# Optimization experiments

Measured on AMD Instinct MI355X. Metric: run time of the kernel, lower is better.

## Reference

```python
import jax, jax.numpy as jnp
import numpy as np

N, E = 50000, 800000
IN, HID, LAT = 512, 256, 128


def setup_inputs() -> dict:
    key = jax.random.key(0)
    ks = jax.random.split(key, 9)
    x = jax.random.normal(ks[0], (N, IN), dtype=jnp.float32)
    edge_index = jax.random.randint(ks[1], (2, E), 0, N, dtype=jnp.int64)
    edge_attr = jax.random.uniform(ks[2], (E,), dtype=jnp.float32)
    # GCNConv weights (glorot-ish scaling) and biases
    W1 = jax.random.normal(ks[3], (IN, HID), dtype=jnp.float32) / np.sqrt(IN)
    b1 = jnp.zeros((HID,), dtype=jnp.float32)
    W_mu = jax.random.normal(ks[4], (HID, LAT), dtype=jnp.float32) / np.sqrt(HID)
    b_mu = jnp.zeros((LAT,), dtype=jnp.float32)
    W_lv = jax.random.normal(ks[5], (HID, LAT), dtype=jnp.float32) / np.sqrt(HID)
    b_lv = jnp.zeros((LAT,), dtype=jnp.float32)
    return {"x": x, "edge_index": edge_index, "edge_attr": edge_attr,
            "W1": W1, "b1": b1, "W_mu": W_mu, "b_mu": b_mu,
            "W_lv": W_lv, "b_lv": b_lv}


def _gcn_norm(edge_index, edge_attr, num_nodes):
    # GCNConv default: add self-loops (weight 1), symmetric normalization
    loops = jnp.arange(num_nodes, dtype=edge_index.dtype)
    src = jnp.concatenate([edge_index[0], loops])
    dst = jnp.concatenate([edge_index[1], loops])
    w = jnp.concatenate([edge_attr, jnp.ones((num_nodes,), edge_attr.dtype)])
    deg = jax.ops.segment_sum(w, dst, num_segments=num_nodes)
    dis = jnp.where(deg > 0, jax.lax.rsqrt(jnp.maximum(deg, 1e-12)), 0.0)
    norm = dis[src] * w * dis[dst]  # [E + N]
    return src, dst, norm


def reference(x, edge_index, edge_attr, W1, b1, W_mu, b_mu, W_lv, b_lv):
    num_nodes = x.shape[0]
    src, dst, norm = _gcn_norm(edge_index, edge_attr, num_nodes)

    def conv(h, W, b):
        m = h @ W                      # dense transform [N, out]
        msg = m[src] * norm[:, None]   # gather + scale  [E+N, out]
        return jax.ops.segment_sum(msg, dst, num_segments=num_nodes) + b

    hidden = jax.nn.relu(conv(x, W1, b1))
    # Dropout(0.2) is identity in eval mode
    mu = conv(hidden, W_mu, b_mu)
    logvar = conv(hidden, W_lv, b_lv)
    return (mu, logvar)
```

## Files before the change

### kernel.cpp

```cpp
#include <hip/hip_runtime.h>

#define IN_F 512
#define HID_F 256
#define LAT_F 128

typedef __bf16 bf16x8 __attribute__((ext_vector_type(8)));
typedef float floatx4 __attribute__((ext_vector_type(4)));

#define FIX_SCALE 1048576.0f

__device__ __forceinline__ unsigned short f2bf(float f) {
    union { float f; unsigned u; } v; v.f = f;
    unsigned r = (v.u + 0x7fff + ((v.u >> 16) & 1)) >> 16;
    return (unsigned short)r;
}
__device__ __forceinline__ float bf2f(unsigned short h) {
    union { unsigned u; float f; } v; v.u = ((unsigned)h) << 16;
    return v.f;
}


__global__ void prep_all(const float* __restrict__ W1, const float* __restrict__ Wmu,
                         const float* __restrict__ Wlv, unsigned long long* __restrict__ packed,
                         unsigned short* __restrict__ Bf1, unsigned short* __restrict__ Bf2,
                         int N) {
    int t = blockIdx.x * 256 + threadIdx.x;
    if (t < N) packed[t] = (1ULL << 32) | (unsigned long long)(unsigned)FIX_SCALE;
    if (t < HID_F * IN_F) {
        int j = t & 7, l = (t >> 3) & 63, jj = (t >> 9) & 1, ks = (t >> 10) & 15, w = t >> 14;
        int n = w * 32 + jj * 16 + (l & 15);
        int k = ks * 32 + (l >> 4) * 8 + j;
        Bf1[t] = f2bf(W1[(size_t)k * HID_F + n]);
    }
    if (t < HID_F * HID_F) {
        int j = t & 7, l = (t >> 3) & 63, jj = (t >> 9) & 1, ks = (t >> 10) & 7, w = t >> 13;
        int n = w * 32 + jj * 16 + (l & 15);
        int k = ks * 32 + (l >> 4) * 8 + j;
        float v = (n < 128) ? Wmu[(size_t)k * LAT_F + n] : Wlv[(size_t)k * LAT_F + (n - 128)];
        Bf2[t] = f2bf(v);
    }
}


__global__ void edge_deg(const int* __restrict__ ei, const float* __restrict__ attr,
                         unsigned long long* __restrict__ packed, int* __restrict__ slot, int E) {
    int e = blockIdx.x * 256 + threadIdx.x;
    if (e < E) {
        int d = ei[E + e];
        unsigned fw = __float2uint_rn(attr[e] * FIX_SCALE);
        unsigned long long old = atomicAdd(&packed[d], (1ULL << 32) | (unsigned long long)fw);
        slot[e] = (int)(old >> 32);
    }
}


__global__ void scan_blocks(const unsigned long long* __restrict__ packed,
                            float* __restrict__ dis, int* __restrict__ excl,
                            int* __restrict__ blockSums, int N) {
    __shared__ int sdata[256];
    int tid = threadIdx.x;
    int base = blockIdx.x * 1024 + tid * 4;
    int v[4]; int sum = 0;
#pragma unroll
    for (int j = 0; j < 4; ++j) {
        int c = 0;
        if (base + j < N) {
            unsigned long long p = packed[base + j];
            c = (int)(p >> 32);
            float dg = (float)(unsigned)(p & 0xffffffffu) * (1.0f / FIX_SCALE);
            dis[base + j] = dg > 0.f ? rsqrtf(fmaxf(dg, 1e-12f)) : 0.f;
        }
        v[j] = c; sum += c;
    }
    sdata[tid] = sum;
    __syncthreads();
    for (int off = 1; off < 256; off <<= 1) {
        int t = (tid >= off) ? sdata[tid - off] : 0;
        __syncthreads();
        sdata[tid] += t;
        __syncthreads();
    }
    if (tid == 255) blockSums[blockIdx.x] = sdata[255];
    int run = sdata[tid] - sum;
#pragma unroll
    for (int j = 0; j < 4; ++j) { if (base + j < N) excl[base + j] = run; run += v[j]; }
}

__global__ void scan_sums(int* blockSums, int NB) {
    __shared__ int s[64];
    int tid = threadIdx.x;
    int v = (tid < NB) ? blockSums[tid] : 0;
    s[tid] = v;
    __syncthreads();
    for (int off = 1; off < 64; off <<= 1) {
        int t = (tid >= off) ? s[tid - off] : 0;
        __syncthreads();
        s[tid] += t;
        __syncthreads();
    }
    if (tid < NB) blockSums[tid] = s[tid] - v;
}

__global__ void scan_add(int* row_ptr, const int* __restrict__ blockSums, int N, int total) {
    int tid = threadIdx.x;
    int base = blockIdx.x * 1024 + tid * 4;
    int add = blockSums[blockIdx.x];
#pragma unroll
    for (int j = 0; j < 4; ++j) if (base + j < N) row_ptr[base + j] += add;
    if (blockIdx.x == 0 && tid == 0) row_ptr[N] = total;
}


__global__ void fill_csr(const int* __restrict__ ei, const float* __restrict__ attr,
                         const int* __restrict__ slot, const float* __restrict__ dis,
                         const int* __restrict__ row_ptr,
                         int* __restrict__ col, float* __restrict__ val, int E, int N) {
    int e = blockIdx.x * 256 + threadIdx.x;
    if (e >= E + N) return;
    int s, d, sl; float w;
    if (e < E) { s = ei[e]; d = ei[E + e]; w = attr[e]; sl = slot[e]; }
    else       { s = d = e - E; w = 1.0f; sl = 0; }
    int pos = row_ptr[d] + sl;
    col[pos] = s;
    val[pos] = dis[s] * w * dis[d];
}


template <bool ABF16, int KK>
__global__ __launch_bounds__(512, 2) void gemm_breg(const void* __restrict__ Avoid,
                                                    const unsigned short* __restrict__ Bfrag,
                                                    unsigned short* __restrict__ C,
                                                    int M, int ntiles) {
    constexpr int NKS = KK / 32;
    constexpr int S   = KK / 128;
    __shared__ unsigned short As[2][64 * 128];

    int tid = threadIdx.x;
    int wave = tid >> 6, lane = tid & 63;
    int mrow = lane & 15, quad = lane >> 4;

    const unsigned short* Abf = (const unsigned short*)Avoid;
    const float*          Afp = (const float*)Avoid;

    bf16x8 bfr[NKS][2];
#pragma unroll
    for (int ks = 0; ks < NKS; ++ks)
#pragma unroll
        for (int jj = 0; jj < 2; ++jj)
            bfr[ks][jj] = *(const bf16x8*)(Bfrag +
                ((((size_t)wave * NKS + ks) * 2 + jj) * 64 + lane) * 8);

    int c  = tid & 15;
    int r0 = tid >> 4;
    int cs0 = (c ^ (r0 & 7)) << 3;
    int cs1 = (c ^ ((r0 + 32) & 7)) << 3;

    float4 a0, a1, a2, a3;
    uint4  u0, u1;

    auto issue = [&](int t_, int s_) {
        int g0 = t_ * 64 + r0;       if (g0 >= M) g0 = M - 1;
        int g1 = t_ * 64 + r0 + 32;  if (g1 >= M) g1 = M - 1;
        if constexpr (ABF16) {
            u0 = *(const uint4*)(Abf + (size_t)g0 * KK + s_ * 128 + c * 8);
            u1 = *(const uint4*)(Abf + (size_t)g1 * KK + s_ * 128 + c * 8);
        } else {
            const float* p0 = Afp + (size_t)g0 * KK + s_ * 128 + c * 8;
            const float* p1 = Afp + (size_t)g1 * KK + s_ * 128 + c * 8;
            a0 = *(const float4*)p0; a1 = *(const float4*)(p0 + 4);
            a2 = *(const float4*)p1; a3 = *(const float4*)(p1 + 4);
        }
    };

    floatx4 acc[4][2];
#pragma unroll
    for (int i = 0; i < 4; ++i)
#pragma unroll
        for (int jj = 0; jj < 2; ++jj) acc[i][jj] = (floatx4){0.f, 0.f, 0.f, 0.f};

    int tile = blockIdx.x;
    if (tile < ntiles) issue(tile, 0);
    int cur = 0;

    for (; tile < ntiles; tile += gridDim.x) {
#pragma unroll
        for (int s = 0; s < S; ++s) {
            if constexpr (ABF16) {
                *(uint4*)&As[cur][r0 * 128 + cs0] = u0;
                *(uint4*)&As[cur][(r0 + 32) * 128 + cs1] = u1;
            } else {
                unsigned short h0[8] = {f2bf(a0.x), f2bf(a0.y), f2bf(a0.z), f2bf(a0.w),
                                        f2bf(a1.x), f2bf(a1.y), f2bf(a1.z), f2bf(a1.w)};
                unsigned short h1[8] = {f2bf(a2.x), f2bf(a2.y), f2bf(a2.z), f2bf(a2.w),
                                        f2bf(a3.x), f2bf(a3.y), f2bf(a3.z), f2bf(a3.w)};
                *(uint4*)&As[cur][r0 * 128 + cs0] = *(uint4*)h0;
                *(uint4*)&As[cur][(r0 + 32) * 128 + cs1] = *(uint4*)h1;
            }
            if (s + 1 < S) issue(tile, s + 1);
            else if (tile + (int)gridDim.x < ntiles) issue(tile + gridDim.x, 0);

            asm volatile("s_waitcnt lgkmcnt(0)" ::: "memory");
            __builtin_amdgcn_s_barrier();

#pragma unroll
            for (int ks = 0; ks < 4; ++ks) {
#pragma unroll
                for (int i = 0; i < 4; ++i) {
                    int row = i * 16 + mrow;
                    bf16x8 af = *(const bf16x8*)&As[cur][row * 128 +
                                    (((ks * 4 + quad) ^ (row & 7)) << 3)];
#pragma unroll
                    for (int jj = 0; jj < 2; ++jj)
                        acc[i][jj] = __builtin_amdgcn_mfma_f32_16x16x32_bf16(
                            af, bfr[s * 4 + ks][jj], acc[i][jj], 0, 0, 0);
                }
            }
            asm volatile("s_waitcnt lgkmcnt(0)" ::: "memory");
            __builtin_amdgcn_s_barrier();
            cur ^= 1;
        }
#pragma unroll
        for (int i = 0; i < 4; ++i)
#pragma unroll
            for (int jj = 0; jj < 2; ++jj) {
                int colo = wave * 32 + jj * 16 + mrow;
#pragma unroll
                for (int v = 0; v < 4; ++v) {
                    int row = tile * 64 + i * 16 + quad * 4 + v;
                    if (row < M) C[(size_t)row * HID_F + colo] = f2bf(acc[i][jj][v]);
                }
                acc[i][jj] = (floatx4){0.f, 0.f, 0.f, 0.f};
            }
    }
}


__global__ void agg_relu(const unsigned short* __restrict__ m, const int* __restrict__ row_ptr,
                         const int* __restrict__ col, const float* __restrict__ val,
                         const float* __restrict__ bias, unsigned short* __restrict__ hidden,
                         int N) {
    int wave = threadIdx.x >> 6, lane = threadIdx.x & 63;
    int i = blockIdx.x * 4 + wave;
    if (i >= N) return;
    int c0 = lane << 2;
    int p0 = __builtin_amdgcn_readfirstlane(row_ptr[i]);
    int p1 = __builtin_amdgcn_readfirstlane(row_ptr[i + 1]);
    float a0 = 0.f, a1 = 0.f, a2 = 0.f, a3 = 0.f;
    for (int p = p0; p < p1; p += 8) {
        int sj[8]; float wj[8];
#pragma unroll
        for (int j = 0; j < 8; ++j) {
            int q = p + j;
            bool ok = q < p1; if (!ok) q = p1 - 1;
            sj[j] = col[q];
            wj[j] = ok ? val[q] : 0.f;
        }
        ushort4 u[8];
#pragma unroll
        for (int j = 0; j < 8; ++j)
            u[j] = *(const ushort4*)(m + (size_t)sj[j] * HID_F + c0);
#pragma unroll
        for (int j = 0; j < 8; ++j) {
            a0 = fmaf(bf2f(u[j].x), wj[j], a0);
            a1 = fmaf(bf2f(u[j].y), wj[j], a1);
            a2 = fmaf(bf2f(u[j].z), wj[j], a2);
            a3 = fmaf(bf2f(u[j].w), wj[j], a3);
        }
    }
    float4 b = *(const float4*)(bias + c0);
    a0 = fmaxf(a0 + b.x, 0.f); a1 = fmaxf(a1 + b.y, 0.f);
    a2 = fmaxf(a2 + b.z, 0.f); a3 = fmaxf(a3 + b.w, 0.f);
    ushort4 o = make_ushort4(f2bf(a0), f2bf(a1), f2bf(a2), f2bf(a3));
    *(ushort4*)(hidden + (size_t)i * HID_F + c0) = o;
}

__global__ void agg_out(const unsigned short* __restrict__ m, const int* __restrict__ row_ptr,
                        const int* __restrict__ col, const float* __restrict__ val,
                        const float* __restrict__ bmu, const float* __restrict__ blv,
                        float* __restrict__ out, int N) {
    int wave = threadIdx.x >> 6, lane = threadIdx.x & 63;
    int i = blockIdx.x * 4 + wave;
    if (i >= N) return;
    int c0 = lane << 2;
    int p0 = __builtin_amdgcn_readfirstlane(row_ptr[i]);
    int p1 = __builtin_amdgcn_readfirstlane(row_ptr[i + 1]);
    float a0 = 0.f, a1 = 0.f, a2 = 0.f, a3 = 0.f;
    for (int p = p0; p < p1; p += 8) {
        int sj[8]; float wj[8];
#pragma unroll
        for (int j = 0; j < 8; ++j) {
            int q = p + j;
            bool ok = q < p1; if (!ok) q = p1 - 1;
            sj[j] = col[q];
            wj[j] = ok ? val[q] : 0.f;
        }
        ushort4 u[8];
#pragma unroll
        for (int j = 0; j < 8; ++j)
            u[j] = *(const ushort4*)(m + (size_t)sj[j] * HID_F + c0);
#pragma unroll
        for (int j = 0; j < 8; ++j) {
            a0 = fmaf(bf2f(u[j].x), wj[j], a0);
            a1 = fmaf(bf2f(u[j].y), wj[j], a1);
            a2 = fmaf(bf2f(u[j].z), wj[j], a2);
            a3 = fmaf(bf2f(u[j].w), wj[j], a3);
        }
    }
    if (lane < 32) {
        float4 b = *(const float4*)(bmu + c0);
        float4 o = make_float4(a0 + b.x, a1 + b.y, a2 + b.z, a3 + b.w);
        *(float4*)(out + (size_t)i * LAT_F + c0) = o;
    } else {
        int c = c0 - 128;
        float4 b = *(const float4*)(blv + c);
        float4 o = make_float4(a0 + b.x, a1 + b.y, a2 + b.z, a3 + b.w);
        *(float4*)(out + (size_t)(N + i) * LAT_F + c) = o;
    }
}


extern "C" void kernel_launch(void* const* d_in, const int* in_sizes, int n_in,
                              void* d_out, int out_size, void* d_ws, size_t ws_size,
                              hipStream_t stream) {
    const float* x    = (const float*)d_in[0];
    const int*   ei   = (const int*)d_in[1];
    const float* attr = (const float*)d_in[2];
    const float* W1   = (const float*)d_in[3];
    const float* b1   = (const float*)d_in[4];
    const float* Wmu  = (const float*)d_in[5];
    const float* bmu  = (const float*)d_in[6];
    const float* Wlv  = (const float*)d_in[7];
    const float* blv  = (const float*)d_in[8];
    float* out = (float*)d_out;

    const int N  = in_sizes[0] / IN_F;
    const int E  = in_sizes[2];
    const int EN = E + N;

    char* w = (char*)d_ws;
    size_t off = 0;
    auto carve = [&](size_t bytes) -> void* {
        void* p = w + off; off += (bytes + 255) & ~(size_t)255; return p;
    };
    unsigned long long* packed = (unsigned long long*)carve((size_t)N * 8);
    float*          dis       = (float*)carve((size_t)N * 4);
    int*            row_ptr   = (int*)  carve((size_t)(N + 1) * 4);
    int*            blockSums = (int*)  carve(64 * 4);
    int*            slot      = (int*)  carve((size_t)E * 4);
    int*            col       = (int*)  carve((size_t)EN * 4);
    float*          val       = (float*)carve((size_t)EN * 4);
    unsigned short* Bf1       = (unsigned short*)carve((size_t)HID_F * IN_F * 2);
    unsigned short* Bf2       = (unsigned short*)carve((size_t)HID_F * HID_F * 2);
    unsigned short* m         = (unsigned short*)carve((size_t)N * HID_F * 2);
    unsigned short* hidden    = (unsigned short*)carve((size_t)N * HID_F * 2);

    prep_all<<<(HID_F * IN_F + 255) / 256, 256, 0, stream>>>(W1, Wmu, Wlv, packed, Bf1, Bf2, N);

    edge_deg<<<(E + 255) / 256, 256, 0, stream>>>(ei, attr, packed, slot, E);

    int NB = (N + 1023) / 1024;
    scan_blocks<<<NB, 256, 0, stream>>>(packed, dis, row_ptr, blockSums, N);
    scan_sums<<<1, 64, 0, stream>>>(blockSums, NB);
    scan_add<<<NB, 256, 0, stream>>>(row_ptr, blockSums, N, EN);

    fill_csr<<<(EN + 255) / 256, 256, 0, stream>>>(ei, attr, slot, dis, row_ptr, col, val, E, N);

    int ntiles = (N + 63) / 64;
    int ggrid = ntiles < 512 ? ntiles : 512;
    gemm_breg<false, IN_F><<<ggrid, 512, 0, stream>>>(x, Bf1, m, N, ntiles);
    agg_relu<<<(N + 3) / 4, 256, 0, stream>>>(m, row_ptr, col, val, b1, hidden, N);
    gemm_breg<true, HID_F><<<ggrid, 512, 0, stream>>>(hidden, Bf2, m, N, ntiles);
    agg_out<<<(N + 3) / 4, 256, 0, stream>>>(m, row_ptr, col, val, bmu, blv, out, N);
}
```

Before: 407.4 us.

## Store intermediate features in column-sliced layout and aggregate per slice

The GEMM outputs and the hidden activations are now stored as 8 column slabs of 32 features each ([slice][N][32]) instead of row-major [N][256]. The aggregation kernels are replaced by a templated agg_slice kernel: each block handles one slab for 16 nodes, with lanes split across 4 edges and 4 column chunks and a shuffle reduction at the end. The aim is to keep each slab's gather working set (about 3.2 MB) cache-resident so random neighbour reads hit L2 or MALL more often. In exchange each edge's col/val is reloaded once per slice, and each lane now processes one edge at a time rather than eight, which lowers memory-level parallelism per lane.

Result: slower. 435.1 us (+6.8%).

```diff
diff --git a/kernel.cpp b/kernel.cpp
--- a/kernel.cpp
+++ b/kernel.cpp
@@ -6,6 +6,7 @@
 
 typedef __bf16 bf16x8 __attribute__((ext_vector_type(8)));
 typedef float floatx4 __attribute__((ext_vector_type(4)));
+typedef unsigned short u16x8 __attribute__((ext_vector_type(8)));
 
 #define FIX_SCALE 1048576.0f
 
@@ -162,8 +163,9 @@
         int g0 = t_ * 64 + r0;       if (g0 >= M) g0 = M - 1;
         int g1 = t_ * 64 + r0 + 32;  if (g1 >= M) g1 = M - 1;
         if constexpr (ABF16) {
-            u0 = *(const uint4*)(Abf + (size_t)g0 * KK + s_ * 128 + c * 8);
-            u1 = *(const uint4*)(Abf + (size_t)g1 * KK + s_ * 128 + c * 8);
+            int sl = s_ * 4 + (c >> 2), cc = c & 3;
+            u0 = *(const uint4*)(Abf + ((size_t)sl * M + g0) * 32 + cc * 8);
+            u1 = *(const uint4*)(Abf + ((size_t)sl * M + g1) * 32 + cc * 8);
         } else {
             const float* p0 = Afp + (size_t)g0 * KK + s_ * 128 + c * 8;
             const float* p1 = Afp + (size_t)g1 * KK + s_ * 128 + c * 8;
@@ -223,11 +225,11 @@
         for (int i = 0; i < 4; ++i)
 #pragma unroll
             for (int jj = 0; jj < 2; ++jj) {
-                int colo = wave * 32 + jj * 16 + mrow;
 #pragma unroll
                 for (int v = 0; v < 4; ++v) {
                     int row = tile * 64 + i * 16 + quad * 4 + v;
-                    if (row < M) C[(size_t)row * HID_F + colo] = f2bf(acc[i][jj][v]);
+                    if (row < M)
+                        C[((size_t)wave * M + row) * 32 + jj * 16 + mrow] = f2bf(acc[i][jj][v]);
                 }
                 acc[i][jj] = (floatx4){0.f, 0.f, 0.f, 0.f};
             }
@@ -235,86 +237,56 @@
 }
 
 
-__global__ void agg_relu(const unsigned short* __restrict__ m, const int* __restrict__ row_ptr,
-                         const int* __restrict__ col, const float* __restrict__ val,
-                         const float* __restrict__ bias, unsigned short* __restrict__ hidden,
-                         int N) {
+template <bool RELU>
+__global__ __launch_bounds__(256) void agg_slice(const unsigned short* __restrict__ ms,
+                                                 const int* __restrict__ row_ptr,
+                                                 const int* __restrict__ col,
+                                                 const float* __restrict__ val,
+                                                 const float* __restrict__ bA,
+                                                 const float* __restrict__ bB,
+                                                 void* __restrict__ outv, int N) {
+    int f  = blockIdx.x & 7;
+    int rg = blockIdx.x >> 3;
     int wave = threadIdx.x >> 6, lane = threadIdx.x & 63;
-    int i = blockIdx.x * 4 + wave;
-    if (i >= N) return;
-    int c0 = lane << 2;
-    int p0 = __builtin_amdgcn_readfirstlane(row_ptr[i]);
-    int p1 = __builtin_amdgcn_readfirstlane(row_ptr[i + 1]);
-    float a0 = 0.f, a1 = 0.f, a2 = 0.f, a3 = 0.f;
-    for (int p = p0; p < p1; p += 8) {
-        int sj[8]; float wj[8];
-#pragma unroll
-        for (int j = 0; j < 8; ++j) {
-            int q = p + j;
-            bool ok = q < p1; if (!ok) q = p1 - 1;
-            sj[j] = col[q];
-            wj[j] = ok ? val[q] : 0.f;
+    int r = lane >> 4, j = (lane >> 2) & 3, c = lane & 3;
+    int i = rg * 16 + wave * 4 + r;
+    int p0 = 0, p1 = 0;
+    if (i < N) { p0 = row_ptr[i]; p1 = row_ptr[i + 1]; }
+    const unsigned short* slab = ms + (size_t)f * N * 32;
+
+    float acc[8] = {0.f, 0.f, 0.f, 0.f, 0.f, 0.f, 0.f, 0.f};
+    for (int t = 0; __any(p0 + t * 4 < p1); ++t) {
+        int q = p0 + t * 4 + j;
+        bool ok = q < p1;
+        int qq = ok ? q : (p1 > 0 ? p1 - 1 : 0);
+        int e = col[qq];
+        float w = ok ? val[qq] : 0.f;
+        u16x8 u = *(const u16x8*)(slab + (size_t)e * 32 + c * 8);
+#pragma unroll
+        for (int k = 0; k < 8; ++k) acc[k] = fmaf(bf2f(u[k]), w, acc[k]);
+    }
+#pragma unroll
+    for (int k = 0; k < 8; ++k) {
+        acc[k] += __shfl_xor(acc[k], 4);
+        acc[k] += __shfl_xor(acc[k], 8);
+    }
+    if (j == 0 && i < N) {
+        if constexpr (RELU) {
+            const float* bp = bA + f * 32 + c * 8;
+            unsigned short h[8];
+#pragma unroll
+            for (int k = 0; k < 8; ++k) h[k] = f2bf(fmaxf(acc[k] + bp[k], 0.f));
+            *(u16x8*)((unsigned short*)outv + ((size_t)f * N + i) * 32 + c * 8) = *(u16x8*)h;
+        } else {
+            float* out = (float*)outv;
+            const float* bp = (f < 4) ? (bA + f * 32 + c * 8) : (bB + (f - 4) * 32 + c * 8);
+            float* op = (f < 4) ? (out + (size_t)i * LAT_F + f * 32 + c * 8)
+                                : (out + (size_t)(N + i) * LAT_F + (f - 4) * 32 + c * 8);
+            float4 o0 = make_float4(acc[0] + bp[0], acc[1] + bp[1], acc[2] + bp[2], acc[3] + bp[3]);
+            float4 o1 = make_float4(acc[4] + bp[4], acc[5] + bp[5], acc[6] + bp[6], acc[7] + bp[7]);
+            *(float4*)op = o0;
+            *(float4*)(op + 4) = o1;
         }
-        ushort4 u[8];
-#pragma unroll
-        for (int j = 0; j < 8; ++j)
-            u[j] = *(const ushort4*)(m + (size_t)sj[j] * HID_F + c0);
-#pragma unroll
-        for (int j = 0; j < 8; ++j) {
-            a0 = fmaf(bf2f(u[j].x), wj[j], a0);
-            a1 = fmaf(bf2f(u[j].y), wj[j], a1);
-            a2 = fmaf(bf2f(u[j].z), wj[j], a2);
-            a3 = fmaf(bf2f(u[j].w), wj[j], a3);
-        }
-    }
-    float4 b = *(const float4*)(bias + c0);
-    a0 = fmaxf(a0 + b.x, 0.f); a1 = fmaxf(a1 + b.y, 0.f);
-    a2 = fmaxf(a2 + b.z, 0.f); a3 = fmaxf(a3 + b.w, 0.f);
-    ushort4 o = make_ushort4(f2bf(a0), f2bf(a1), f2bf(a2), f2bf(a3));
-    *(ushort4*)(hidden + (size_t)i * HID_F + c0) = o;
-}
-
-__global__ void agg_out(const unsigned short* __restrict__ m, const int* __restrict__ row_ptr,
-                        const int* __restrict__ col, const float* __restrict__ val,
-                        const float* __restrict__ bmu, const float* __restrict__ blv,
-                        float* __restrict__ out, int N) {
-    int wave = threadIdx.x >> 6, lane = threadIdx.x & 63;
-    int i = blockIdx.x * 4 + wave;
-    if (i >= N) return;
-    int c0 = lane << 2;
-    int p0 = __builtin_amdgcn_readfirstlane(row_ptr[i]);
-    int p1 = __builtin_amdgcn_readfirstlane(row_ptr[i + 1]);
-    float a0 = 0.f, a1 = 0.f, a2 = 0.f, a3 = 0.f;
-    for (int p = p0; p < p1; p += 8) {
-        int sj[8]; float wj[8];
-#pragma unroll
-        for (int j = 0; j < 8; ++j) {
-            int q = p + j;
-            bool ok = q < p1; if (!ok) q = p1 - 1;
-            sj[j] = col[q];
-            wj[j] = ok ? val[q] : 0.f;
-        }
-        ushort4 u[8];
-#pragma unroll
-        for (int j = 0; j < 8; ++j)
-            u[j] = *(const ushort4*)(m + (size_t)sj[j] * HID_F + c0);
-#pragma unroll
-        for (int j = 0; j < 8; ++j) {
-            a0 = fmaf(bf2f(u[j].x), wj[j], a0);
-            a1 = fmaf(bf2f(u[j].y), wj[j], a1);
-            a2 = fmaf(bf2f(u[j].z), wj[j], a2);
-            a3 = fmaf(bf2f(u[j].w), wj[j], a3);
-        }
-    }
-    if (lane < 32) {
-        float4 b = *(const float4*)(bmu + c0);
-        float4 o = make_float4(a0 + b.x, a1 + b.y, a2 + b.z, a3 + b.w);
-        *(float4*)(out + (size_t)i * LAT_F + c0) = o;
-    } else {
-        int c = c0 - 128;
-        float4 b = *(const float4*)(blv + c);
-        float4 o = make_float4(a0 + b.x, a1 + b.y, a2 + b.z, a3 + b.w);
-        *(float4*)(out + (size_t)(N + i) * LAT_F + c) = o;
     }
 }
 
@@ -367,8 +339,9 @@
 
     int ntiles = (N + 63) / 64;
     int ggrid = ntiles < 512 ? ntiles : 512;
+    int agrid = ((N + 15) / 16) * 8;
     gemm_breg<false, IN_F><<<ggrid, 512, 0, stream>>>(x, Bf1, m, N, ntiles);
-    agg_relu<<<(N + 3) / 4, 256, 0, stream>>>(m, row_ptr, col, val, b1, hidden, N);
+    agg_slice<true><<<agrid, 256, 0, stream>>>(m, row_ptr, col, val, b1, nullptr, hidden, N);
     gemm_breg<true, HID_F><<<ggrid, 512, 0, stream>>>(hidden, Bf2, m, N, ntiles);
-    agg_out<<<(N + 3) / 4, 256, 0, stream>>>(m, row_ptr, col, val, bmu, blv, out, N);
-}
+    agg_slice<false><<<agrid, 256, 0, stream>>>(m, row_ptr, col, val, bmu, blv, out, N);
+}
```

## Split aggregation kernels into two column-half passes with two nodes per wave

Applied to the files above, without the earlier changes.

Each aggregation kernel now runs twice, once per 128-column half of the feature matrix. Each wave processes two nodes with 32 lanes apiece, so the gathered working set per pass is half as large and may fit better in cache. The cost is reading the CSR structure twice and having the two half-waves diverge when their nodes have different degrees. The readfirstlane scalarization of the row pointers is dropped.

Result: slower. 419.0 us (+2.8%).

```diff
diff --git a/kernel.cpp b/kernel.cpp
--- a/kernel.cpp
+++ b/kernel.cpp
@@ -235,16 +235,16 @@
 }
 
 
-__global__ void agg_relu(const unsigned short* __restrict__ m, const int* __restrict__ row_ptr,
-                         const int* __restrict__ col, const float* __restrict__ val,
-                         const float* __restrict__ bias, unsigned short* __restrict__ hidden,
-                         int N) {
+__global__ void agg_relu_h(const unsigned short* __restrict__ m, const int* __restrict__ row_ptr,
+                           const int* __restrict__ col, const float* __restrict__ val,
+                           const float* __restrict__ bias, unsigned short* __restrict__ hidden,
+                           int N, int half) {
     int wave = threadIdx.x >> 6, lane = threadIdx.x & 63;
-    int i = blockIdx.x * 4 + wave;
+    int r = lane >> 5, l5 = lane & 31;
+    int i = blockIdx.x * 8 + wave * 2 + r;
     if (i >= N) return;
-    int c0 = lane << 2;
-    int p0 = __builtin_amdgcn_readfirstlane(row_ptr[i]);
-    int p1 = __builtin_amdgcn_readfirstlane(row_ptr[i + 1]);
+    int c0 = half * 128 + l5 * 4;
+    int p0 = row_ptr[i], p1 = row_ptr[i + 1];
     float a0 = 0.f, a1 = 0.f, a2 = 0.f, a3 = 0.f;
     for (int p = p0; p < p1; p += 8) {
         int sj[8]; float wj[8];
@@ -274,16 +274,17 @@
     *(ushort4*)(hidden + (size_t)i * HID_F + c0) = o;
 }
 
-__global__ void agg_out(const unsigned short* __restrict__ m, const int* __restrict__ row_ptr,
-                        const int* __restrict__ col, const float* __restrict__ val,
-                        const float* __restrict__ bmu, const float* __restrict__ blv,
-                        float* __restrict__ out, int N) {
+__global__ void agg_out_h(const unsigned short* __restrict__ m, const int* __restrict__ row_ptr,
+                          const int* __restrict__ col, const float* __restrict__ val,
+                          const float* __restrict__ bhalf, float* __restrict__ out,
+                          int N, int half) {
     int wave = threadIdx.x >> 6, lane = threadIdx.x & 63;
-    int i = blockIdx.x * 4 + wave;
+    int r = lane >> 5, l5 = lane & 31;
+    int i = blockIdx.x * 8 + wave * 2 + r;
     if (i >= N) return;
-    int c0 = lane << 2;
-    int p0 = __builtin_amdgcn_readfirstlane(row_ptr[i]);
-    int p1 = __builtin_amdgcn_readfirstlane(row_ptr[i + 1]);
+    int cc = l5 * 4;
+    int c0 = half * 128 + cc;
+    int p0 = row_ptr[i], p1 = row_ptr[i + 1];
     float a0 = 0.f, a1 = 0.f, a2 = 0.f, a3 = 0.f;
     for (int p = p0; p < p1; p += 8) {
         int sj[8]; float wj[8];
@@ -306,16 +307,10 @@
             a3 = fmaf(bf2f(u[j].w), wj[j], a3);
         }
     }
-    if (lane < 32) {
-        float4 b = *(const float4*)(bmu + c0);
-        float4 o = make_float4(a0 + b.x, a1 + b.y, a2 + b.z, a3 + b.w);
-        *(float4*)(out + (size_t)i * LAT_F + c0) = o;
-    } else {
-        int c = c0 - 128;
-        float4 b = *(const float4*)(blv + c);
-        float4 o = make_float4(a0 + b.x, a1 + b.y, a2 + b.z, a3 + b.w);
-        *(float4*)(out + (size_t)(N + i) * LAT_F + c) = o;
-    }
+    float4 b = *(const float4*)(bhalf + cc);
+    float4 o = make_float4(a0 + b.x, a1 + b.y, a2 + b.z, a3 + b.w);
+    size_t row = half ? (size_t)(N + i) : (size_t)i;
+    *(float4*)(out + row * LAT_F + cc) = o;
 }
 
 
@@ -367,8 +362,11 @@
 
     int ntiles = (N + 63) / 64;
     int ggrid = ntiles < 512 ? ntiles : 512;
+    int agrid = (N + 7) / 8;
     gemm_breg<false, IN_F><<<ggrid, 512, 0, stream>>>(x, Bf1, m, N, ntiles);
-    agg_relu<<<(N + 3) / 4, 256, 0, stream>>>(m, row_ptr, col, val, b1, hidden, N);
+    agg_relu_h<<<agrid, 256, 0, stream>>>(m, row_ptr, col, val, b1, hidden, N, 0);
+    agg_relu_h<<<agrid, 256, 0, stream>>>(m, row_ptr, col, val, b1, hidden, N, 1);
     gemm_breg<true, HID_F><<<ggrid, 512, 0, stream>>>(hidden, Bf2, m, N, ntiles);
-    agg_out<<<(N + 3) / 4, 256, 0, stream>>>(m, row_ptr, col, val, bmu, blv, out, N);
-}
+    agg_out_h<<<agrid, 256, 0, stream>>>(m, row_ptr, col, val, bmu, out, N, 0);
+    agg_out_h<<<agrid, 256, 0, stream>>>(m, row_ptr, col, val, blv, out, N, 1);
+}
```

## Fuse first-layer aggregation with ReLU into second-layer GEMM via LDS tiles

Applied to the files above, without the earlier changes.

Replaces the separate agg_relu kernel and the second GEMM with one persistent kernel. Each block aggregates 64 rows of neighbor features, applies bias and ReLU, and writes the bf16 hidden tile into swizzled LDS. It then runs MFMA against register-resident weight fragments to produce the second transform. This removes the global write and read of the hidden matrix and one launch. In exchange the grid is capped at 512 blocks, so fewer waves are available to hide gather latency, and gather depth drops from 8 to 4 edges per batch.

New measurement: 416.0 us. 1.02x slower.

```diff
diff --git a/kernel.cpp b/kernel.cpp
--- a/kernel.cpp
+++ b/kernel.cpp
@@ -235,44 +235,111 @@
 }
 
 
-__global__ void agg_relu(const unsigned short* __restrict__ m, const int* __restrict__ row_ptr,
-                         const int* __restrict__ col, const float* __restrict__ val,
-                         const float* __restrict__ bias, unsigned short* __restrict__ hidden,
-                         int N) {
-    int wave = threadIdx.x >> 6, lane = threadIdx.x & 63;
-    int i = blockIdx.x * 4 + wave;
-    if (i >= N) return;
-    int c0 = lane << 2;
-    int p0 = __builtin_amdgcn_readfirstlane(row_ptr[i]);
-    int p1 = __builtin_amdgcn_readfirstlane(row_ptr[i + 1]);
-    float a0 = 0.f, a1 = 0.f, a2 = 0.f, a3 = 0.f;
-    for (int p = p0; p < p1; p += 8) {
-        int sj[8]; float wj[8];
-#pragma unroll
-        for (int j = 0; j < 8; ++j) {
-            int q = p + j;
-            bool ok = q < p1; if (!ok) q = p1 - 1;
-            sj[j] = col[q];
-            wj[j] = ok ? val[q] : 0.f;
-        }
-        ushort4 u[8];
-#pragma unroll
-        for (int j = 0; j < 8; ++j)
-            u[j] = *(const ushort4*)(m + (size_t)sj[j] * HID_F + c0);
-#pragma unroll
-        for (int j = 0; j < 8; ++j) {
-            a0 = fmaf(bf2f(u[j].x), wj[j], a0);
-            a1 = fmaf(bf2f(u[j].y), wj[j], a1);
-            a2 = fmaf(bf2f(u[j].z), wj[j], a2);
-            a3 = fmaf(bf2f(u[j].w), wj[j], a3);
-        }
-    }
-    float4 b = *(const float4*)(bias + c0);
-    a0 = fmaxf(a0 + b.x, 0.f); a1 = fmaxf(a1 + b.y, 0.f);
-    a2 = fmaxf(a2 + b.z, 0.f); a3 = fmaxf(a3 + b.w, 0.f);
-    ushort4 o = make_ushort4(f2bf(a0), f2bf(a1), f2bf(a2), f2bf(a3));
-    *(ushort4*)(hidden + (size_t)i * HID_F + c0) = o;
-}
+__global__ __launch_bounds__(512, 4) void agg_gemm2(
+        const unsigned short* __restrict__ m1, const int* __restrict__ row_ptr,
+        const int* __restrict__ col, const float* __restrict__ val,
+        const float* __restrict__ b1, const unsigned short* __restrict__ Bfrag,
+        unsigned short* __restrict__ m2, int M, int ntiles) {
+    constexpr int NKS = 8;
+    __shared__ unsigned short As[2][64 * 128];
+
+    int tid = threadIdx.x;
+    int wave = tid >> 6, lane = tid & 63;
+    int mrow = lane & 15, quad = lane >> 4;
+
+    bf16x8 bfr[NKS][2];
+#pragma unroll
+    for (int ks = 0; ks < NKS; ++ks)
+#pragma unroll
+        for (int jj = 0; jj < 2; ++jj)
+            bfr[ks][jj] = *(const bf16x8*)(Bfrag +
+                ((((size_t)wave * NKS + ks) * 2 + jj) * 64 + lane) * 8);
+
+    int c0   = lane << 2;
+    int s_w  = lane >> 5;
+    int kk_w = (lane & 31) >> 1;
+    int hw_w = (lane & 1) << 2;
+
+    floatx4 acc[4][2];
+#pragma unroll
+    for (int i = 0; i < 4; ++i)
+#pragma unroll
+        for (int jj = 0; jj < 2; ++jj) acc[i][jj] = (floatx4){0.f, 0.f, 0.f, 0.f};
+
+    for (int tile = blockIdx.x; tile < ntiles; tile += gridDim.x) {
+#pragma unroll 1
+        for (int rr = 0; rr < 8; ++rr) {
+            int i = tile * 64 + wave * 8 + rr;
+            float a0 = 0.f, a1 = 0.f, a2 = 0.f, a3 = 0.f;
+            if (i < M) {
+                int p0 = __builtin_amdgcn_readfirstlane(row_ptr[i]);
+                int p1 = __builtin_amdgcn_readfirstlane(row_ptr[i + 1]);
+                for (int p = p0; p < p1; p += 4) {
+                    int sj[4]; float wj[4];
+#pragma unroll
+                    for (int j = 0; j < 4; ++j) {
+                        int q = p + j;
+                        bool ok = q < p1; if (!ok) q = p1 - 1;
+                        sj[j] = col[q];
+                        wj[j] = ok ? val[q] : 0.f;
+                    }
+                    ushort4 u[4];
+#pragma unroll
+                    for (int j = 0; j < 4; ++j)
+                        u[j] = *(const ushort4*)(m1 + (size_t)sj[j] * HID_F + c0);
+#pragma unroll
+                    for (int j = 0; j < 4; ++j) {
+                        a0 = fmaf(bf2f(u[j].x), wj[j], a0);
+                        a1 = fmaf(bf2f(u[j].y), wj[j], a1);
+                        a2 = fmaf(bf2f(u[j].z), wj[j], a2);
+                        a3 = fmaf(bf2f(u[j].w), wj[j], a3);
+                    }
+                }
+                float4 b = *(const float4*)(b1 + c0);
+                a0 = fmaxf(a0 + b.x, 0.f); a1 = fmaxf(a1 + b.y, 0.f);
+                a2 = fmaxf(a2 + b.z, 0.f); a3 = fmaxf(a3 + b.w, 0.f);
+            }
+            int r = wave * 8 + rr;
+            unsigned h01 = ((unsigned)f2bf(a1) << 16) | f2bf(a0);
+            unsigned h23 = ((unsigned)f2bf(a3) << 16) | f2bf(a2);
+            uint2 pk = make_uint2(h01, h23);
+            *(uint2*)&As[s_w][r * 128 + ((kk_w ^ (r & 7)) << 3) + hw_w] = pk;
+        }
+        asm volatile("s_waitcnt lgkmcnt(0)" ::: "memory");
+        __builtin_amdgcn_s_barrier();
+
+#pragma unroll
+        for (int s = 0; s < 2; ++s)
+#pragma unroll
+            for (int ks = 0; ks < 4; ++ks)
+#pragma unroll
+                for (int i = 0; i < 4; ++i) {
+                    int row = i * 16 + mrow;
+                    bf16x8 af = *(const bf16x8*)&As[s][row * 128 +
+                                    (((ks * 4 + quad) ^ (row & 7)) << 3)];
+#pragma unroll
+                    for (int jj = 0; jj < 2; ++jj)
+                        acc[i][jj] = __builtin_amdgcn_mfma_f32_16x16x32_bf16(
+                            af, bfr[s * 4 + ks][jj], acc[i][jj], 0, 0, 0);
+                }
+        asm volatile("s_waitcnt lgkmcnt(0)" ::: "memory");
+        __builtin_amdgcn_s_barrier();
+
+#pragma unroll
+        for (int i = 0; i < 4; ++i)
+#pragma unroll
+            for (int jj = 0; jj < 2; ++jj) {
+                int colo = wave * 32 + jj * 16 + mrow;
+#pragma unroll
+                for (int v = 0; v < 4; ++v) {
+                    int row = tile * 64 + i * 16 + quad * 4 + v;
+                    if (row < M) m2[(size_t)row * HID_F + colo] = f2bf(acc[i][jj][v]);
+                }
+                acc[i][jj] = (floatx4){0.f, 0.f, 0.f, 0.f};
+            }
+    }
+}
+
 
 __global__ void agg_out(const unsigned short* __restrict__ m, const int* __restrict__ row_ptr,
                         const int* __restrict__ col, const float* __restrict__ val,
@@ -351,8 +418,8 @@
     float*          val       = (float*)carve((size_t)EN * 4);
     unsigned short* Bf1       = (unsigned short*)carve((size_t)HID_F * IN_F * 2);
     unsigned short* Bf2       = (unsigned short*)carve((size_t)HID_F * HID_F * 2);
-    unsigned short* m         = (unsigned short*)carve((size_t)N * HID_F * 2);
-    unsigned short* hidden    = (unsigned short*)carve((size_t)N * HID_F * 2);
+    unsigned short* m1        = (unsigned short*)carve((size_t)N * HID_F * 2);
+    unsigned short* m2        = (unsigned short*)carve((size_t)N * HID_F * 2);
 
     prep_all<<<(HID_F * IN_F + 255) / 256, 256, 0, stream>>>(W1, Wmu, Wlv, packed, Bf1, Bf2, N);
 
@@ -367,8 +434,7 @@
 
     int ntiles = (N + 63) / 64;
     int ggrid = ntiles < 512 ? ntiles : 512;
-    gemm_breg<false, IN_F><<<ggrid, 512, 0, stream>>>(x, Bf1, m, N, ntiles);
-    agg_relu<<<(N + 3) / 4, 256, 0, stream>>>(m, row_ptr, col, val, b1, hidden, N);
-    gemm_breg<true, HID_F><<<ggrid, 512, 0, stream>>>(hidden, Bf2, m, N, ntiles);
-    agg_out<<<(N + 3) / 4, 256, 0, stream>>>(m, row_ptr, col, val, bmu, blv, out, N);
-}
+    gemm_breg<false, IN_F><<<ggrid, 512, 0, stream>>>(x, Bf1, m1, N, ntiles);
+    agg_gemm2<<<ggrid, 512, 0, stream>>>(m1, row_ptr, col, val, b1, Bf2, m2, N, ntiles);
+    agg_out<<<(N + 3) / 4, 256, 0, stream>>>(m2, row_ptr, col, val, bmu, blv, out, N);
+}
```
